# Performance work log

Measured on AMD Instinct MI355X. Metric: run time of the kernel, lower is better.

## Reference

```python
import jax, jax.numpy as jnp
import numpy as np

D = 1024
H = 16
HD = D // H
MLP = 4 * D
EPS = 1e-5


def layernorm(x, g, b):
    mu = jnp.mean(x, axis=-1, keepdims=True)
    var = jnp.mean(jnp.square(x - mu), axis=-1, keepdims=True)
    return (x - mu) * jax.lax.rsqrt(var + EPS) * g + b


def setup_inputs() -> dict:
    key = jax.random.key(0)
    ks = jax.random.split(key, 12)
    s = 0.02
    return {
        "x": jax.random.normal(ks[0], (2, 2048, D), jnp.float32),
        "ln1_g": jnp.ones((D,), jnp.float32),
        "ln1_b": jnp.zeros((D,), jnp.float32),
        "lnm_g": jnp.ones((D,), jnp.float32),
        "lnm_b": jnp.zeros((D,), jnp.float32),
        "qkv_w": jax.random.normal(ks[1], (D, 3 * D), jnp.float32) * s,
        "qkv_b": jnp.zeros((3 * D,), jnp.float32),
        "proj_w": jax.random.normal(ks[2], (D, D), jnp.float32) * s,
        "proj_b": jnp.zeros((D,), jnp.float32),
        "fc1_w": jax.random.normal(ks[3], (D, MLP), jnp.float32) * s,
        "fc1_b": jnp.zeros((MLP,), jnp.float32),
        "fc2_w": jax.random.normal(ks[4], (MLP, D), jnp.float32) * s,
        "fc2_b": jnp.zeros((D,), jnp.float32),
    }


def reference(x, ln1_g, ln1_b, lnm_g, lnm_b, qkv_w, qkv_b, proj_w, proj_b,
              fc1_w, fc1_b, fc2_w, fc2_b):
    B, N, _ = x.shape
    scale = HD ** -0.5
    # --- self-attention on norm1(x) ---
    h = layernorm(x, ln1_g, ln1_b)
    qkv = h @ qkv_w + qkv_b                       # [B, N, 3D]
    qkv = qkv.reshape(B, N, 3, H, HD)
    q, k, v = qkv[:, :, 0], qkv[:, :, 1], qkv[:, :, 2]  # [B, N, H, HD]
    attn = jnp.einsum("bqhd,bkhd->bhqk", q, k) * scale
    attn = jax.nn.softmax(attn, axis=-1)
    o = jnp.einsum("bhqk,bkhd->bqhd", attn, v).reshape(B, N, D)
    x = x + (o @ proj_w + proj_b)
    # --- MLP ---
    m = layernorm(x, lnm_g, lnm_b)
    m = jax.nn.gelu(m @ fc1_w + fc1_b, approximate=False)
    x = x + (m @ fc2_w + fc2_b)
    return x
```

## Files before the change

kernel.cpp:

```cpp
#include <hip/hip_runtime.h>

typedef __bf16 bf16_t;
typedef bf16_t bf16x4 __attribute__((ext_vector_type(4)));
typedef bf16_t bf16x8 __attribute__((ext_vector_type(8)));
typedef float f32x4 __attribute__((ext_vector_type(4)));
typedef unsigned short u16x8 __attribute__((ext_vector_type(8)));

#define MFMA(a, b, c) __builtin_amdgcn_mfma_f32_16x16x32_bf16(a, b, c, 0, 0, 0)

__device__ inline float exp2_fast(float x) {
  float r;
  asm volatile("v_exp_f32 %0, %1" : "=v"(r) : "v"(x));
  return r;
}

__device__ inline void gll16(const bf16_t* g, bf16_t* l) {
  __builtin_amdgcn_global_load_lds(
      (const __attribute__((address_space(1))) unsigned int*)(g),
      (__attribute__((address_space(3))) unsigned int*)(l), 16, 0, 0);
}

__device__ inline float gelu_f(float v) {
  float ax = fabsf(v) * 0.70710678118f;
  float t = __builtin_amdgcn_rcpf(1.0f + 0.3275911f * ax);
  float p = ((((1.061405429f * t - 1.453152027f) * t + 1.421413741f) * t -
              0.284496736f) * t + 0.254829592f) * t;
  float e = exp2_fast(-ax * ax * 1.4426950408889634f);
  float erf = 1.0f - p * e;
  erf = v < 0.f ? -erf : erf;
  return 0.5f * v * (1.0f + erf);
}

__global__ __launch_bounds__(256) void ln_kernel(const float* __restrict__ x,
                                                 const float* __restrict__ g,
                                                 const float* __restrict__ b,
                                                 bf16_t* __restrict__ out) {
  long row = blockIdx.x;
  const float4* xr = (const float4*)(x + row * 1024);
  float4 v = xr[threadIdx.x];
  float s = v.x + v.y + v.z + v.w;
  float s2 = v.x * v.x + v.y * v.y + v.z * v.z + v.w * v.w;
#pragma unroll
  for (int m = 32; m >= 1; m >>= 1) {
    s += __shfl_xor(s, m);
    s2 += __shfl_xor(s2, m);
  }
  __shared__ float red[8];
  int wid = threadIdx.x >> 6;
  if ((threadIdx.x & 63) == 0) {
    red[wid] = s;
    red[4 + wid] = s2;
  }
  __syncthreads();
  s = red[0] + red[1] + red[2] + red[3];
  s2 = red[4] + red[5] + red[6] + red[7];
  float mu = s * (1.f / 1024.f);
  float rs = rsqrtf(s2 * (1.f / 1024.f) - mu * mu + 1e-5f);
  float4 gv = ((const float4*)g)[threadIdx.x];
  float4 bv = ((const float4*)b)[threadIdx.x];
  bf16_t o0 = (bf16_t)((v.x - mu) * rs * gv.x + bv.x);
  bf16_t o1 = (bf16_t)((v.y - mu) * rs * gv.y + bv.y);
  bf16_t o2 = (bf16_t)((v.z - mu) * rs * gv.z + bv.z);
  bf16_t o3 = (bf16_t)((v.w - mu) * rs * gv.w + bv.w);
  ushort4 pk;
  pk.x = *(unsigned short*)&o0;
  pk.y = *(unsigned short*)&o1;
  pk.z = *(unsigned short*)&o2;
  pk.w = *(unsigned short*)&o3;
  *(ushort4*)(out + row * 1024 + threadIdx.x * 4) = pk;
}

__global__ __launch_bounds__(256) void wconv_all(
    const float* __restrict__ qkv_w, bf16_t* __restrict__ qkv_wt,
    const float* __restrict__ proj_w, bf16_t* __restrict__ proj_wt,
    const float* __restrict__ fc1_w, bf16_t* __restrict__ fc1_wt,
    const float* __restrict__ fc2_w, bf16_t* __restrict__ fc2_wt) {
  int id = blockIdx.x;
  const float* W;
  bf16_t* Wt;
  int K, N, bx, by;
  if (id < 768) {
    W = qkv_w; Wt = qkv_wt; K = 1024; N = 3072; bx = id % 48; by = id / 48;
  } else if (id < 1024) {
    int l = id - 768;
    W = proj_w; Wt = proj_wt; K = 1024; N = 1024; bx = l % 16; by = l / 16;
  } else if (id < 2048) {
    int l = id - 1024;
    W = fc1_w; Wt = fc1_wt; K = 1024; N = 4096; bx = l % 64; by = l / 64;
  } else {
    int l = id - 2048;
    W = fc2_w; Wt = fc2_wt; K = 4096; N = 1024; bx = l % 16; by = l / 16;
  }
  __shared__ float t[64][65];
  int n0 = bx * 64, k0 = by * 64;
  int tid = threadIdx.x;
  int c4 = tid & 15;
  int r = tid >> 4;
#pragma unroll
  for (int s = 0; s < 4; s++) {
    int k = r + s * 16;
    float4 v = *(const float4*)(W + (long)(k0 + k) * N + n0 + c4 * 4);
    t[k][c4 * 4] = v.x;
    t[k][c4 * 4 + 1] = v.y;
    t[k][c4 * 4 + 2] = v.z;
    t[k][c4 * 4 + 3] = v.w;
  }
  __syncthreads();
  int n = tid >> 2;
  int kc = (tid & 3) * 16;
  ushort4 pk[4];
#pragma unroll
  for (int c = 0; c < 4; c++) {
#pragma unroll
    for (int j = 0; j < 4; j++) {
      bf16_t x = (bf16_t)t[kc + c * 4 + j][n];
      ((unsigned short*)&pk[c])[j] = *(unsigned short*)&x;
    }
  }
  bf16_t* dst = Wt + (long)(n0 + n) * K + k0 + kc;
#pragma unroll
  for (int c = 0; c < 4; c++) *(ushort4*)(dst + c * 4) = pk[c];
}

#define STAGE_PTR(DA, DB, k0)                 \
  gll16(ga + (k0), DA + w * 512);             \
  gll16(ga + (k0) + astep, DA + 4096 + w * 512); \
  gll16(gb + (k0), DB + w * 512);

#define COMPUTE(LA, LB)                                                \
  {                                                                    \
    bf16x8 af[4], bfr[4];                                              \
    _Pragma("unroll") for (int mt = 0; mt < 4; mt++) af[mt] =          \
        *(const bf16x8*)(LA + (wm + mt * 16 + l15) * 32 + quad * 8);   \
    _Pragma("unroll") for (int nt = 0; nt < 4; nt++) bfr[nt] =         \
        *(const bf16x8*)(LB + (wn + nt * 16 + l15) * 32 + quad * 8);   \
    _Pragma("unroll") for (int mt = 0; mt < 4; mt++)                   \
        _Pragma("unroll") for (int nt = 0; nt < 4; nt++) acc[mt][nt] = \
            MFMA(af[mt], bfr[nt], acc[mt][nt]);                        \
  }

#define WB3 asm volatile("s_waitcnt vmcnt(3)\ns_barrier" ::: "memory")
#define WB0 asm volatile("s_waitcnt vmcnt(0)\ns_barrier" ::: "memory")

__global__ __launch_bounds__(512, 4) void gemm_kernel(
    const bf16_t* __restrict__ A, const bf16_t* __restrict__ Bt,
    const float* __restrict__ bias, const float* __restrict__ resid,
    void* __restrict__ Cout, int M, int N, int K, int epi) {
  __shared__ bf16_t lA0[256 * 32], lB0[128 * 32];
  __shared__ bf16_t lA1[256 * 32], lB1[128 * 32];
  __shared__ bf16_t lA2[256 * 32], lB2[128 * 32];
  int tid = threadIdx.x;
  int bn = blockIdx.x, bm = blockIdx.y;
  int kchunk = K / gridDim.z;
  int kbeg = blockIdx.z * kchunk, kend = kbeg + kchunk;

  int lane = tid & 63, w = tid >> 6;
  int quad = lane >> 4, l15 = lane & 15;
  int wm = (w & 3) * 64, wn = (w >> 2) * 64;

  f32x4 acc[4][4];
#pragma unroll
  for (int i = 0; i < 4; i++)
#pragma unroll
    for (int j = 0; j < 4; j++) acc[i][j] = (f32x4){0.f, 0.f, 0.f, 0.f};

  const bf16_t* ga = A + (long)(bm * 256 + w * 16 + (lane >> 2)) * K + (lane & 3) * 8;
  const bf16_t* gb = Bt + (long)(bn * 128 + w * 16 + (lane >> 2)) * K + (lane & 3) * 8;
  long astep = (long)128 * K;

  int nit = (kend - kbeg) >> 5;
  bf16_t *A0 = lA0, *A1 = lA1, *A2 = lA2;
  bf16_t *B0 = lB0, *B1 = lB1, *B2 = lB2;
  STAGE_PTR(A0, B0, kbeg);
  STAGE_PTR(A1, B1, kbeg + 32);
  for (int i = 0; i < nit; i++) {
    if (i + 1 < nit) { WB3; } else { WB0; }
    if (i + 2 < nit) {
      int ks = kbeg + (i + 2) * 32;
      STAGE_PTR(A2, B2, ks);
    }
    COMPUTE(A0, B0);
    bf16_t* t;
    t = A0; A0 = A1; A1 = A2; A2 = t;
    t = B0; B0 = B1; B1 = B2; B2 = t;
  }

#pragma unroll
  for (int mt = 0; mt < 4; mt++) {
#pragma unroll
    for (int r = 0; r < 4; r++) {
      long row = bm * 256 + wm + mt * 16 + quad * 4 + r;
#pragma unroll
      for (int nt = 0; nt < 4; nt++) {
        int col = bn * 128 + wn + nt * 16 + l15;
        long idx = row * N + col;
        if (epi == 3) {
          ((bf16_t*)Cout)[(long)blockIdx.z * M * N + idx] = (bf16_t)acc[mt][nt][r];
        } else {
          float v = acc[mt][nt][r] + bias[col];
          if (epi == 1) {
            ((float*)Cout)[idx] = v + resid[idx];
          } else if (epi == 2) {
            ((bf16_t*)Cout)[idx] = (bf16_t)gelu_f(v);
          } else {
            ((bf16_t*)Cout)[idx] = (bf16_t)v;
          }
        }
      }
    }
  }
}

__global__ __launch_bounds__(256) void reduce_ln_kernel(
    const bf16_t* __restrict__ p, const float* __restrict__ bias,
    const float* __restrict__ resid, float* __restrict__ x1,
    const float* __restrict__ g, const float* __restrict__ bb,
    bf16_t* __restrict__ mb) {
  const long MN = (long)4096 * 1024;
  long row = blockIdx.x;
  int t = threadIdx.x;
  bf16x4 a0 = *(const bf16x4*)(p + row * 1024 + t * 4);
  bf16x4 a1 = *(const bf16x4*)(p + MN + row * 1024 + t * 4);
  bf16x4 a2 = *(const bf16x4*)(p + 2 * MN + row * 1024 + t * 4);
  bf16x4 a3 = *(const bf16x4*)(p + 3 * MN + row * 1024 + t * 4);
  float4 r = ((const float4*)(resid + row * 1024))[t];
  float4 bv = ((const float4*)bias)[t];
  float4 v;
  v.x = (float)a0[0] + (float)a1[0] + (float)a2[0] + (float)a3[0] + r.x + bv.x;
  v.y = (float)a0[1] + (float)a1[1] + (float)a2[1] + (float)a3[1] + r.y + bv.y;
  v.z = (float)a0[2] + (float)a1[2] + (float)a2[2] + (float)a3[2] + r.z + bv.z;
  v.w = (float)a0[3] + (float)a1[3] + (float)a2[3] + (float)a3[3] + r.w + bv.w;
  ((float4*)(x1 + row * 1024))[t] = v;
  float s = v.x + v.y + v.z + v.w;
  float s2 = v.x * v.x + v.y * v.y + v.z * v.z + v.w * v.w;
#pragma unroll
  for (int m = 32; m >= 1; m >>= 1) {
    s += __shfl_xor(s, m);
    s2 += __shfl_xor(s2, m);
  }
  __shared__ float red[8];
  int wid = t >> 6;
  if ((t & 63) == 0) {
    red[wid] = s;
    red[4 + wid] = s2;
  }
  __syncthreads();
  s = red[0] + red[1] + red[2] + red[3];
  s2 = red[4] + red[5] + red[6] + red[7];
  float mu = s * (1.f / 1024.f);
  float rs = rsqrtf(s2 * (1.f / 1024.f) - mu * mu + 1e-5f);
  float4 gv = ((const float4*)g)[t];
  float4 b2 = ((const float4*)bb)[t];
  bf16_t o0 = (bf16_t)((v.x - mu) * rs * gv.x + b2.x);
  bf16_t o1 = (bf16_t)((v.y - mu) * rs * gv.y + b2.y);
  bf16_t o2 = (bf16_t)((v.z - mu) * rs * gv.z + b2.z);
  bf16_t o3 = (bf16_t)((v.w - mu) * rs * gv.w + b2.w);
  ushort4 pk;
  pk.x = *(unsigned short*)&o0;
  pk.y = *(unsigned short*)&o1;
  pk.z = *(unsigned short*)&o2;
  pk.w = *(unsigned short*)&o3;
  *(ushort4*)(mb + row * 1024 + t * 4) = pk;
}

__global__ __launch_bounds__(256) void reduce4_kernel(const bf16_t* __restrict__ p,
                                                      const float* __restrict__ bias,
                                                      const float* __restrict__ resid,
                                                      float* __restrict__ out) {
  long i = (long)blockIdx.x * 256 + threadIdx.x;
  const long MN = (long)4096 * 1024;
  bf16x4 a0 = *(const bf16x4*)(p + i * 4);
  bf16x4 a1 = *(const bf16x4*)(p + MN + i * 4);
  bf16x4 a2 = *(const bf16x4*)(p + 2 * MN + i * 4);
  bf16x4 a3 = *(const bf16x4*)(p + 3 * MN + i * 4);
  float4 r = ((const float4*)resid)[i];
  float4 bv = ((const float4*)bias)[i & 255];
  float4 o;
  o.x = (float)a0[0] + (float)a1[0] + (float)a2[0] + (float)a3[0] + r.x + bv.x;
  o.y = (float)a0[1] + (float)a1[1] + (float)a2[1] + (float)a3[1] + r.y + bv.y;
  o.z = (float)a0[2] + (float)a1[2] + (float)a2[2] + (float)a3[2] + r.z + bv.z;
  o.w = (float)a0[3] + (float)a1[3] + (float)a2[3] + (float)a3[3] + r.w + bv.w;
  ((float4*)out)[i] = o;
}

#define LDV 72

__global__ __launch_bounds__(256) void attn_kernel(const bf16_t* __restrict__ qkv,
                                                   bf16_t* __restrict__ o) {
  const int LD = 3072;
  int id = blockIdx.x;
  int within = id >> 3;
  int bh = (id & 7) * 4 + (within >> 4);
  int qt = within & 15;
  int h = bh & 15, b = bh >> 4;

  int tid = threadIdx.x, w = tid >> 6, lane = tid & 63;
  int quad = lane >> 4, l15 = lane & 15;
  int qrow = qt * 128 + w * 32;
  const bf16_t* base = qkv + (long)b * 2048 * LD + h * 64;
  const bf16_t* Qp = base;
  const bf16_t* Kp = base + 1024;
  const bf16_t* Vp = base + 2048;

  __shared__ bf16_t lK[2][64 * 64];
  __shared__ bf16_t lV[2][64 * LDV];
  __shared__ bf16_t lP[4][32 * LDV];
  bf16_t* myp = lP[w];

  const bf16_t* kg =
      Kp + (long)(w * 16 + (lane >> 3)) * LD + (((lane & 7) ^ (lane >> 3)) & 7) * 8;
  int kk = tid & 31;
  int d0 = (tid >> 5) * 8;
  const bf16_t* vg = Vp + (long)(2 * kk) * LD + d0;

  gll16(kg, lK[0] + w * 1024);
  gll16(kg + 8 * (long)LD, lK[0] + w * 1024 + 512);
  u16x8 va = *(const u16x8*)(vg);
  u16x8 vb = *(const u16x8*)(vg + LD);

  bf16x8 qf[2][2];
#pragma unroll
  for (int qi = 0; qi < 2; qi++)
#pragma unroll
    for (int d = 0; d < 2; d++)
      qf[qi][d] =
          *(const bf16x8*)(Qp + (long)(qrow + qi * 16 + l15) * LD + d * 32 + quad * 8);

  f32x4 oacc[2][4];
#pragma unroll
  for (int qi = 0; qi < 2; qi++)
#pragma unroll
    for (int t = 0; t < 4; t++) oacc[qi][t] = (f32x4){0.f, 0.f, 0.f, 0.f};
  float li_p[2][4] = {{0.f, 0.f, 0.f, 0.f}, {0.f, 0.f, 0.f, 0.f}};
  const float c2 = 0.18033688011112042f;

  int sw0 = (quad ^ l15) & 7;
  int sw1 = ((quad + 4) ^ l15) & 7;

  for (int it = 0; it < 32; it++) {
    int cur = it & 1, nxt = cur ^ 1;
    asm volatile("s_waitcnt vmcnt(0)\ns_barrier" ::: "memory");
    unsigned int* lvw = (unsigned int*)lV[cur];
#pragma unroll
    for (int j = 0; j < 8; j++)
      lvw[(d0 + j) * (LDV / 2) + kk] = (unsigned int)va[j] | ((unsigned int)vb[j] << 16);
    u16x8 va_n = va, vb_n = vb;
    if (it + 1 < 32) {
      long koff2 = (long)(it + 1) * 64 * LD;
      gll16(kg + koff2, lK[nxt] + w * 1024);
      gll16(kg + koff2 + 8 * (long)LD, lK[nxt] + w * 1024 + 512);
      va_n = *(const u16x8*)(vg + koff2);
      vb_n = *(const u16x8*)(vg + koff2 + LD);
    }
    asm volatile("s_waitcnt lgkmcnt(0)\ns_barrier" ::: "memory");

    bf16x8 kf[4][2];
#pragma unroll
    for (int st = 0; st < 4; st++) {
      const bf16_t* krow = lK[cur] + (st * 16 + l15) * 64;
      kf[st][0] = *(const bf16x8*)(krow + sw0 * 8);
      kf[st][1] = *(const bf16x8*)(krow + sw1 * 8);
    }
    f32x4 s[2][4];
#pragma unroll
    for (int qi = 0; qi < 2; qi++)
#pragma unroll
      for (int st = 0; st < 4; st++) {
        f32x4 z = (f32x4){0.f, 0.f, 0.f, 0.f};
        z = MFMA(qf[qi][0], kf[st][0], z);
        s[qi][st] = MFMA(qf[qi][1], kf[st][1], z);
      }

#pragma unroll
    for (int qi = 0; qi < 2; qi++)
#pragma unroll
      for (int st = 0; st < 4; st++)
#pragma unroll
        for (int r = 0; r < 4; r++) {
          float p = exp2_fast(s[qi][st][r] * c2);
          s[qi][st][r] = p;
          li_p[qi][r] += p;
        }

#pragma unroll
    for (int qi = 0; qi < 2; qi++)
#pragma unroll
      for (int r = 0; r < 4; r++)
#pragma unroll
        for (int st = 0; st < 4; st++)
          myp[(qi * 16 + quad * 4 + r) * LDV + st * 16 + l15] = (bf16_t)s[qi][st][r];
    asm volatile("s_waitcnt lgkmcnt(0)" ::: "memory");

    bf16x8 pa[2][2];
#pragma unroll
    for (int qi = 0; qi < 2; qi++) {
      pa[qi][0] = *(const bf16x8*)(myp + (qi * 16 + l15) * LDV + quad * 8);
      pa[qi][1] = *(const bf16x8*)(myp + (qi * 16 + l15) * LDV + 32 + quad * 8);
    }
#pragma unroll
    for (int t = 0; t < 4; t++) {
      const bf16_t* vr = lV[cur] + (t * 16 + l15) * LDV + quad * 8;
      bf16x8 v0 = *(const bf16x8*)(vr);
      bf16x8 v1 = *(const bf16x8*)(vr + 32);
#pragma unroll
      for (int qi = 0; qi < 2; qi++) {
        oacc[qi][t] = MFMA(pa[qi][0], v0, oacc[qi][t]);
        oacc[qi][t] = MFMA(pa[qi][1], v1, oacc[qi][t]);
      }
    }
    va = va_n;
    vb = vb_n;
  }

#pragma unroll
  for (int qi = 0; qi < 2; qi++) {
    float li[4];
#pragma unroll
    for (int r = 0; r < 4; r++) {
      float s = li_p[qi][r];
#pragma unroll
      for (int x = 8; x >= 1; x >>= 1) s += __shfl_xor(s, x);
      li[r] = s;
    }
#pragma unroll
    for (int t = 0; t < 4; t++)
#pragma unroll
      for (int r = 0; r < 4; r++) {
        long q = qrow + qi * 16 + quad * 4 + r;
        o[((long)b * 2048 + q) * 1024 + h * 64 + t * 16 + l15] =
            (bf16_t)(oacc[qi][t][r] / li[r]);
      }
  }
}

extern "C" void kernel_launch(void* const* d_in, const int* in_sizes, int n_in,
                              void* d_out, int out_size, void* d_ws, size_t ws_size,
                              hipStream_t stream) {
  (void)in_sizes; (void)n_in; (void)out_size; (void)ws_size;
  const float* x = (const float*)d_in[0];
  const float* ln1_g = (const float*)d_in[1];
  const float* ln1_b = (const float*)d_in[2];
  const float* lnm_g = (const float*)d_in[3];
  const float* lnm_b = (const float*)d_in[4];
  const float* qkv_w = (const float*)d_in[5];
  const float* qkv_b = (const float*)d_in[6];
  const float* proj_w = (const float*)d_in[7];
  const float* proj_b = (const float*)d_in[8];
  const float* fc1_w = (const float*)d_in[9];
  const float* fc1_b = (const float*)d_in[10];
  const float* fc2_w = (const float*)d_in[11];
  const float* fc2_b = (const float*)d_in[12];
  float* out = (float*)d_out;

  const int M = 4096;
  const int D_ = 1024, MLP_ = 4096, QKV = 3072;

  char* ws = (char*)d_ws;
  bf16_t* h = (bf16_t*)(ws);
  bf16_t* qkvb = (bf16_t*)(ws + (8u << 20));
  bf16_t* ob = (bf16_t*)(ws + (32u << 20));
  float* x1 = (float*)(ws + (40u << 20));
  bf16_t* mb = (bf16_t*)(ws + (56u << 20));
  bf16_t* gb = (bf16_t*)(ws + (64u << 20));
  bf16_t* qkv_wt = (bf16_t*)(ws + (96u << 20));
  bf16_t* proj_wt = (bf16_t*)(ws + (102u << 20));
  bf16_t* fc1_wt = (bf16_t*)(ws + (104u << 20));
  bf16_t* fc2_wt = (bf16_t*)(ws + (112u << 20));
  bf16_t* p_proj = (bf16_t*)(ws);
  bf16_t* p_fc2 = (bf16_t*)(ws);

  wconv_all<<<3072, 256, 0, stream>>>(qkv_w, qkv_wt, proj_w, proj_wt, fc1_w, fc1_wt,
                                      fc2_w, fc2_wt);

  ln_kernel<<<M, 256, 0, stream>>>(x, ln1_g, ln1_b, h);
  gemm_kernel<<<dim3(QKV / 128, M / 256), 512, 0, stream>>>(h, qkv_wt, qkv_b, nullptr,
                                                            qkvb, M, QKV, D_, 0);
  attn_kernel<<<512, 256, 0, stream>>>(qkvb, ob);
  gemm_kernel<<<dim3(D_ / 128, M / 256, 4), 512, 0, stream>>>(ob, proj_wt, nullptr,
                                                              nullptr, p_proj, M, D_,
                                                              D_, 3);
  reduce_ln_kernel<<<M, 256, 0, stream>>>(p_proj, proj_b, x, x1, lnm_g, lnm_b, mb);
  gemm_kernel<<<dim3(MLP_ / 128, M / 256), 512, 0, stream>>>(mb, fc1_wt, fc1_b,
                                                             nullptr, gb, M, MLP_, D_,
                                                             2);
  gemm_kernel<<<dim3(D_ / 128, M / 256, 4), 512, 0, stream>>>(gb, fc2_wt, nullptr,
                                                              nullptr, p_fc2, M, D_,
                                                              MLP_, 3);
  reduce4_kernel<<<4096, 256, 0, stream>>>(p_fc2, fc2_b, x1, out);
}
```

Baseline: 390.9 us.

## Fuse LN1 into weight-convert launch, XCD-aware GEMM tile mapping, prescale Q

The first layernorm now runs as extra blocks inside the weight-conversion kernel, which removes one launch and lets the two overlap. GEMM kernels switch to a flat 1D grid remapped so that blocks sharing a column tile (and its k-split) land on the same XCD, aiming at better L2 reuse of the B tiles. The attention kernel folds the softmax scale into Q once at load, dropping a multiply per score. Scaling Q in bf16 adds a little rounding.

```diff
diff --git a/kernel.cpp b/kernel.cpp
--- a/kernel.cpp
+++ b/kernel.cpp
@@ -31,51 +31,50 @@
   return 0.5f * v * (1.0f + erf);
 }
 
-__global__ __launch_bounds__(256) void ln_kernel(const float* __restrict__ x,
-                                                 const float* __restrict__ g,
-                                                 const float* __restrict__ b,
-                                                 bf16_t* __restrict__ out) {
-  long row = blockIdx.x;
-  const float4* xr = (const float4*)(x + row * 1024);
-  float4 v = xr[threadIdx.x];
-  float s = v.x + v.y + v.z + v.w;
-  float s2 = v.x * v.x + v.y * v.y + v.z * v.z + v.w * v.w;
-#pragma unroll
-  for (int m = 32; m >= 1; m >>= 1) {
-    s += __shfl_xor(s, m);
-    s2 += __shfl_xor(s2, m);
-  }
-  __shared__ float red[8];
-  int wid = threadIdx.x >> 6;
-  if ((threadIdx.x & 63) == 0) {
-    red[wid] = s;
-    red[4 + wid] = s2;
-  }
-  __syncthreads();
-  s = red[0] + red[1] + red[2] + red[3];
-  s2 = red[4] + red[5] + red[6] + red[7];
-  float mu = s * (1.f / 1024.f);
-  float rs = rsqrtf(s2 * (1.f / 1024.f) - mu * mu + 1e-5f);
-  float4 gv = ((const float4*)g)[threadIdx.x];
-  float4 bv = ((const float4*)b)[threadIdx.x];
-  bf16_t o0 = (bf16_t)((v.x - mu) * rs * gv.x + bv.x);
-  bf16_t o1 = (bf16_t)((v.y - mu) * rs * gv.y + bv.y);
-  bf16_t o2 = (bf16_t)((v.z - mu) * rs * gv.z + bv.z);
-  bf16_t o3 = (bf16_t)((v.w - mu) * rs * gv.w + bv.w);
-  ushort4 pk;
-  pk.x = *(unsigned short*)&o0;
-  pk.y = *(unsigned short*)&o1;
-  pk.z = *(unsigned short*)&o2;
-  pk.w = *(unsigned short*)&o3;
-  *(ushort4*)(out + row * 1024 + threadIdx.x * 4) = pk;
-}
-
 __global__ __launch_bounds__(256) void wconv_all(
     const float* __restrict__ qkv_w, bf16_t* __restrict__ qkv_wt,
     const float* __restrict__ proj_w, bf16_t* __restrict__ proj_wt,
     const float* __restrict__ fc1_w, bf16_t* __restrict__ fc1_wt,
-    const float* __restrict__ fc2_w, bf16_t* __restrict__ fc2_wt) {
+    const float* __restrict__ fc2_w, bf16_t* __restrict__ fc2_wt,
+    const float* __restrict__ x, const float* __restrict__ g1,
+    const float* __restrict__ b1, bf16_t* __restrict__ h) {
   int id = blockIdx.x;
+  if (id >= 3072) {
+    long row = id - 3072;
+    const float4* xr = (const float4*)(x + row * 1024);
+    float4 v = xr[threadIdx.x];
+    float s = v.x + v.y + v.z + v.w;
+    float s2 = v.x * v.x + v.y * v.y + v.z * v.z + v.w * v.w;
+#pragma unroll
+    for (int m = 32; m >= 1; m >>= 1) {
+      s += __shfl_xor(s, m);
+      s2 += __shfl_xor(s2, m);
+    }
+    __shared__ float red[8];
+    int wid = threadIdx.x >> 6;
+    if ((threadIdx.x & 63) == 0) {
+      red[wid] = s;
+      red[4 + wid] = s2;
+    }
+    __syncthreads();
+    s = red[0] + red[1] + red[2] + red[3];
+    s2 = red[4] + red[5] + red[6] + red[7];
+    float mu = s * (1.f / 1024.f);
+    float rs = rsqrtf(s2 * (1.f / 1024.f) - mu * mu + 1e-5f);
+    float4 gv = ((const float4*)g1)[threadIdx.x];
+    float4 bv = ((const float4*)b1)[threadIdx.x];
+    bf16_t o0 = (bf16_t)((v.x - mu) * rs * gv.x + bv.x);
+    bf16_t o1 = (bf16_t)((v.y - mu) * rs * gv.y + bv.y);
+    bf16_t o2 = (bf16_t)((v.z - mu) * rs * gv.z + bv.z);
+    bf16_t o3 = (bf16_t)((v.w - mu) * rs * gv.w + bv.w);
+    ushort4 pk;
+    pk.x = *(unsigned short*)&o0;
+    pk.y = *(unsigned short*)&o1;
+    pk.z = *(unsigned short*)&o2;
+    pk.w = *(unsigned short*)&o3;
+    *(ushort4*)(h + row * 1024 + threadIdx.x * 4) = pk;
+    return;
+  }
   const float* W;
   bf16_t* Wt;
   int K, N, bx, by;
@@ -113,8 +112,8 @@
   for (int c = 0; c < 4; c++) {
 #pragma unroll
     for (int j = 0; j < 4; j++) {
-      bf16_t x = (bf16_t)t[kc + c * 4 + j][n];
-      ((unsigned short*)&pk[c])[j] = *(unsigned short*)&x;
+      bf16_t xq = (bf16_t)t[kc + c * 4 + j][n];
+      ((unsigned short*)&pk[c])[j] = *(unsigned short*)&xq;
     }
   }
   bf16_t* dst = Wt + (long)(n0 + n) * K + k0 + kc;
@@ -145,14 +144,21 @@
 __global__ __launch_bounds__(512, 4) void gemm_kernel(
     const bf16_t* __restrict__ A, const bf16_t* __restrict__ Bt,
     const float* __restrict__ bias, const float* __restrict__ resid,
-    void* __restrict__ Cout, int M, int N, int K, int epi) {
+    void* __restrict__ Cout, int M, int N, int K, int epi, int nbn, int nz) {
   __shared__ bf16_t lA0[256 * 32], lB0[128 * 32];
   __shared__ bf16_t lA1[256 * 32], lB1[128 * 32];
   __shared__ bf16_t lA2[256 * 32], lB2[128 * 32];
   int tid = threadIdx.x;
-  int bn = blockIdx.x, bm = blockIdx.y;
-  int kchunk = K / gridDim.z;
-  int kbeg = blockIdx.z * kchunk, kend = kbeg + kchunk;
+  int id = blockIdx.x;
+  int xcd = id & 7;
+  int slot = id >> 3;
+  int gpx = (nbn * nz) >> 3;
+  int g = xcd * gpx + (slot >> 4);
+  int bm = slot & 15;
+  int bn = g / nz;
+  int kz = g % nz;
+  int kchunk = K / nz;
+  int kbeg = kz * kchunk, kend = kbeg + kchunk;
 
   int lane = tid & 63, w = tid >> 6;
   int quad = lane >> 4, l15 = lane & 15;
@@ -195,7 +201,7 @@
         int col = bn * 128 + wn + nt * 16 + l15;
         long idx = row * N + col;
         if (epi == 3) {
-          ((bf16_t*)Cout)[(long)blockIdx.z * M * N + idx] = (bf16_t)acc[mt][nt][r];
+          ((bf16_t*)Cout)[(long)kz * M * N + idx] = (bf16_t)acc[mt][nt][r];
         } else {
           float v = acc[mt][nt][r] + bias[col];
           if (epi == 1) {
@@ -318,13 +324,17 @@
   u16x8 va = *(const u16x8*)(vg);
   u16x8 vb = *(const u16x8*)(vg + LD);
 
+  const float c2 = 0.18033688011112042f;
   bf16x8 qf[2][2];
 #pragma unroll
   for (int qi = 0; qi < 2; qi++)
 #pragma unroll
-    for (int d = 0; d < 2; d++)
-      qf[qi][d] =
+    for (int d = 0; d < 2; d++) {
+      bf16x8 q0 =
           *(const bf16x8*)(Qp + (long)(qrow + qi * 16 + l15) * LD + d * 32 + quad * 8);
+#pragma unroll
+      for (int j = 0; j < 8; j++) qf[qi][d][j] = (bf16_t)((float)q0[j] * c2);
+    }
 
   f32x4 oacc[2][4];
 #pragma unroll
@@ -332,7 +342,6 @@
 #pragma unroll
     for (int t = 0; t < 4; t++) oacc[qi][t] = (f32x4){0.f, 0.f, 0.f, 0.f};
   float li_p[2][4] = {{0.f, 0.f, 0.f, 0.f}, {0.f, 0.f, 0.f, 0.f}};
-  const float c2 = 0.18033688011112042f;
 
   int sw0 = (quad ^ l15) & 7;
   int sw1 = ((quad + 4) ^ l15) & 7;
@@ -377,7 +386,7 @@
       for (int st = 0; st < 4; st++)
 #pragma unroll
         for (int r = 0; r < 4; r++) {
-          float p = exp2_fast(s[qi][st][r] * c2);
+          float p = exp2_fast(s[qi][st][r]);
           s[qi][st][r] = p;
           li_p[qi][r] += p;
         }
@@ -469,22 +478,17 @@
   bf16_t* p_proj = (bf16_t*)(ws);
   bf16_t* p_fc2 = (bf16_t*)(ws);
 
-  wconv_all<<<3072, 256, 0, stream>>>(qkv_w, qkv_wt, proj_w, proj_wt, fc1_w, fc1_wt,
-                                      fc2_w, fc2_wt);
-
-  ln_kernel<<<M, 256, 0, stream>>>(x, ln1_g, ln1_b, h);
-  gemm_kernel<<<dim3(QKV / 128, M / 256), 512, 0, stream>>>(h, qkv_wt, qkv_b, nullptr,
-                                                            qkvb, M, QKV, D_, 0);
+  wconv_all<<<7168, 256, 0, stream>>>(qkv_w, qkv_wt, proj_w, proj_wt, fc1_w, fc1_wt,
+                                      fc2_w, fc2_wt, x, ln1_g, ln1_b, h);
+  gemm_kernel<<<384, 512, 0, stream>>>(h, qkv_wt, qkv_b, nullptr, qkvb, M, QKV, D_, 0,
+                                       24, 1);
   attn_kernel<<<512, 256, 0, stream>>>(qkvb, ob);
-  gemm_kernel<<<dim3(D_ / 128, M / 256, 4), 512, 0, stream>>>(ob, proj_wt, nullptr,
-                                                              nullptr, p_proj, M, D_,
-                                                              D_, 3);
+  gemm_kernel<<<512, 512, 0, stream>>>(ob, proj_wt, nullptr, nullptr, p_proj, M, D_,
+                                       D_, 3, 8, 4);
   reduce_ln_kernel<<<M, 256, 0, stream>>>(p_proj, proj_b, x, x1, lnm_g, lnm_b, mb);
-  gemm_kernel<<<dim3(MLP_ / 128, M / 256), 512, 0, stream>>>(mb, fc1_wt, fc1_b,
-                                                             nullptr, gb, M, MLP_, D_,
-                                                             2);
-  gemm_kernel<<<dim3(D_ / 128, M / 256, 4), 512, 0, stream>>>(gb, fc2_wt, nullptr,
-                                                              nullptr, p_fc2, M, D_,
-                                                              MLP_, 3);
+  gemm_kernel<<<512, 512, 0, stream>>>(mb, fc1_wt, fc1_b, nullptr, gb, M, MLP_, D_, 2,
+                                       32, 1);
+  gemm_kernel<<<512, 512, 0, stream>>>(gb, fc2_wt, nullptr, nullptr, p_fc2, M, D_,
+                                       MLP_, 3, 8, 4);
   reduce4_kernel<<<4096, 256, 0, stream>>>(p_fc2, fc2_b, x1, out);
 }
```

Measured after the change: 384.6 us. Within noise of the previous version (-1.6%).
